# Optimization experiments

Measured on AMD Instinct MI355X. Metric: run time of the kernel, lower is better.

The kernel has to match this reference:

```python
import jax, jax.numpy as jnp
import numpy as np

# dims
D_IN, D, H, HD = 1536, 256, 8, 32
DEPTH, FFN = 2, 1024
B, L = 1, 8191
NGRIDS, TILE = 256, 256
SEGMENTS = [1024, 2048, 4096, 8192, 16384]   # get_optimal_segment_length(32768, 256)
RATIOS = [1, 2, 4, 8, 16]                    # LongNet canonical dilation ratios
SCALE = HD ** -0.5


def setup_inputs() -> dict:
    key = jax.random.key(0)
    ks = jax.random.split(key, 16)
    w = lambda k, s: jax.random.normal(k, s, jnp.float32) * 0.02
    return {
        "x": jax.random.normal(ks[0], (B, L, D_IN), jnp.float32),
        "coords": jax.random.randint(ks[1], (B, L, 2), 0, NGRIDS * TILE, jnp.int32),
        "proj_w": w(ks[2], (D_IN, D)), "proj_b": jnp.zeros((D,), jnp.float32),
        "cls_tok": w(ks[3], (1, 1, D)),
        "Wq": w(ks[4], (DEPTH, D, D)), "Wk": w(ks[5], (DEPTH, D, D)),
        "Wv": w(ks[6], (DEPTH, D, D)), "Wo": w(ks[7], (DEPTH, D, D)),
        "bq": jnp.zeros((DEPTH, D), jnp.float32), "bk": jnp.zeros((DEPTH, D), jnp.float32),
        "bv": jnp.zeros((DEPTH, D), jnp.float32), "bo": jnp.zeros((DEPTH, D), jnp.float32),
        "ln1_g": jnp.ones((DEPTH, D), jnp.float32), "ln1_b": jnp.zeros((DEPTH, D), jnp.float32),
        "ln2_g": jnp.ones((DEPTH, D), jnp.float32), "ln2_b": jnp.zeros((DEPTH, D), jnp.float32),
        "W1": w(ks[8], (DEPTH, D, FFN)), "b1": jnp.zeros((DEPTH, FFN), jnp.float32),
        "W2": w(ks[9], (DEPTH, FFN, D)), "b2": jnp.zeros((DEPTH, D), jnp.float32),
        "enc_g": jnp.ones((D,), jnp.float32), "enc_b": jnp.zeros((D,), jnp.float32),
        "norm_g": jnp.ones((D,), jnp.float32), "norm_b": jnp.zeros((D,), jnp.float32),
    }


def _ln(x, g, b):
    mu = x.mean(-1, keepdims=True)
    v = ((x - mu) ** 2).mean(-1, keepdims=True)
    return (x - mu) * jax.lax.rsqrt(v + 1e-5) * g + b


def _pos_table():
    # MAE-style 2D sincos pos embed, row 0 = cls (zeros). [NGRIDS^2+1, D]
    g = jnp.arange(NGRIDS, dtype=jnp.float32)
    gw, gh = jnp.meshgrid(g, g)  # gw[i,j]=j, gh[i,j]=i; flatten index = i*NGRIDS + j
    def one(pos):
        omega = 1.0 / (10000.0 ** (jnp.arange(D // 4, dtype=jnp.float32) / (D // 4)))
        o = pos.reshape(-1)[:, None] * omega[None]
        return jnp.concatenate([jnp.sin(o), jnp.cos(o)], -1)
    tab = jnp.concatenate([one(gw), one(gh)], -1)
    return jnp.concatenate([jnp.zeros((1, D), jnp.float32), tab], 0)


def _dilated_attn(q, k, v):
    # q,k,v: [B,S,H,HD]. LongNet: per (segment w, dilation r) branch, sparse in-segment
    # attention on stride-r rows (head-dependent offset h%r), branches fused via their
    # softmax log-sum-exp weights.
    S = q.shape[1]
    hh = jnp.arange(H)[:, None]
    outs, lses = [], []
    for w, r in zip(SEGMENTS, RATIOS):
        n = (S + w - 1) // w
        Sp = n * w
        def seg(t):
            tp = jnp.pad(t, ((0, 0), (0, Sp - S), (0, 0), (0, 0)))
            return tp.reshape(B, n, w, H, HD).transpose(0, 1, 3, 2, 4)  # [B,n,H,w,HD]
        qs_, ks_, vs_ = seg(q), seg(k), seg(v)
        t = w // r
        idx = (hh % r) + r * jnp.arange(t)[None, :]                  # [H,t]
        qs = qs_[:, :, hh, idx]                                      # [B,n,H,t,HD]
        ks = ks_[:, :, hh, idx]
        vs = vs_[:, :, hh, idx]
        valid = (jnp.arange(n)[:, None, None] * w + idx[None]) < S   # [n,H,t]
        sc = jnp.einsum('bnhtd,bnhsd->bnhts', qs, ks) * SCALE
        sc = jnp.where(valid[None, :, :, None, :], sc, -1e9)
        m = sc.max(-1, keepdims=True)
        p = jnp.exp(sc - m)
        den = p.sum(-1, keepdims=True)
        o = jnp.einsum('bnhts,bnhsd->bnhtd', p, vs) / den
        lse = m[..., 0] + jnp.log(den[..., 0])                       # [B,n,H,t]
        fo = jnp.zeros((B, n, H, w, HD), q.dtype).at[:, :, hh, idx].set(o)
        fl = jnp.full((B, n, H, w), -1e30, q.dtype).at[:, :, hh, idx].set(lse)
        outs.append(fo.transpose(0, 1, 3, 2, 4).reshape(B, Sp, H, HD)[:, :S])
        lses.append(fl.transpose(0, 1, 3, 2).reshape(B, Sp, H)[:, :S])
    Ls = jnp.stack(lses)   # [5,B,S,H]
    Os = jnp.stack(outs)   # [5,B,S,H,HD]
    wts = jnp.exp(Ls - Ls.max(0, keepdims=True))
    return (wts[..., None] * Os).sum(0) / wts.sum(0)[..., None]


def _forward(x, coords, proj_w, proj_b, cls_tok, Wq, Wk, Wv, Wo, bq, bk, bv, bo,
             ln1_g, ln1_b, ln2_g, ln2_b, W1, b1, W2, b2, enc_g, enc_b, norm_g, norm_b):
    h = x @ proj_w + proj_b                                   # patch embed [B,L,D]
    tab = _pos_table()
    cg = jnp.floor(coords.astype(jnp.float32) / TILE).astype(jnp.int32)
    pos = cg[..., 0] * NGRIDS + cg[..., 1] + 1                # coords_to_pos
    h = h + tab[pos]
    cls = jnp.broadcast_to(cls_tok + tab[0], (B, 1, D))
    h = jnp.concatenate([cls, h], 1)                          # [B,S,D], S = L+1
    S = h.shape[1]
    for i in range(DEPTH):                                    # pre-LN LongNet encoder layers
        a = _ln(h, ln1_g[i], ln1_b[i])
        q = (a @ Wq[i] + bq[i]).reshape(B, S, H, HD)
        k = (a @ Wk[i] + bk[i]).reshape(B, S, H, HD)
        v = (a @ Wv[i] + bv[i]).reshape(B, S, H, HD)
        o = _dilated_attn(q, k, v).reshape(B, S, D)
        h = h + o @ Wo[i] + bo[i]
        f = _ln(h, ln2_g[i], ln2_b[i])
        h = h + jax.nn.gelu(f @ W1[i] + b1[i], approximate=False) @ W2[i] + b2[i]
    h = _ln(h, enc_g, enc_b)     # encoder final LN
    h = _ln(h, norm_g, norm_b)   # model self.norm
    return h[:, 0]               # cls embedding (global_pool=False)


def reference(x, coords, proj_w, proj_b, cls_tok, Wq, Wk, Wv, Wo, bq, bk, bv, bo,
              ln1_g, ln1_b, ln2_g, ln2_b, W1, b1, W2, b2, enc_g, enc_b, norm_g, norm_b):
    return _forward(x, coords, proj_w, proj_b, cls_tok, Wq, Wk, Wv, Wo, bq, bk, bv, bo,
                    ln1_g, ln1_b, ln2_g, ln2_b, W1, b1, W2, b2, enc_g, enc_b, norm_g, norm_b)
```

## Files before the change

### kernel.cpp

```cpp
#include <hip/hip_runtime.h>
#include <math.h>

#define S_TOT 8192
#define DD 256
#define NHEAD 8
#define HDSZ 32
#define ATT_SCALE 0.17677669529663687f
#define ATT_SCALE_LOG2E 0.25506601f

typedef short short8 __attribute__((ext_vector_type(8)));
typedef short short4v __attribute__((ext_vector_type(4)));
typedef float f32x4 __attribute__((ext_vector_type(4)));
typedef unsigned short ushort;

#define OFF_PROJ 0
#define OFF_WQ0  393216
#define OFF_WK0  458752
#define OFF_WV0  524288
#define OFF_WO0  589824
#define OFF_W10  655360
#define OFF_W20  917504
#define OFF_WK1  1179648
#define OFF_WV1  1245184
#define OFF_WQ1  1310720
#define OFF_WO1  1376256
#define OFF_W11  1441792
#define OFF_W21  1703936
#define WBUF_TOT 1966080

__device__ inline ushort f2bf(float f) {
    union { float f; unsigned u; } c; c.f = f;
    unsigned u = c.u;
    u += 0x7fffu + ((u >> 16) & 1u);
    return (ushort)(u >> 16);
}
__device__ inline float bf2f(ushort u) {
    union { unsigned u; float f; } c; c.u = ((unsigned)u) << 16;
    return c.f;
}
__device__ inline float gelu_exact(float v) {
    return 0.5f * v * (1.0f + erff(v * 0.7071067811865475f));
}
__device__ inline unsigned cvtpk_bf16(float a, float b) {
    unsigned r;
    asm("v_cvt_pk_bf16_f32 %0, %1, %2" : "=v"(r) : "v"(a), "v"(b));
    return r;
}
__device__ inline short8 cat44(short4v a, short4v b) {
    return __builtin_shufflevector(a, b, 0, 1, 2, 3, 4, 5, 6, 7);
}
__device__ inline float block_sum256(float v, float* red) {
    #pragma unroll
    for (int off = 32; off > 0; off >>= 1) v += __shfl_down(v, off, 64);
    const int wid = threadIdx.x >> 6, lane = threadIdx.x & 63;
    if (lane == 0) red[wid] = v;
    __syncthreads();
    const float s = red[0] + red[1] + red[2] + red[3];
    __syncthreads();
    return s;
}

__global__ __launch_bounds__(256)
void setup_kernel(const float* __restrict__ x, const float* __restrict__ proj_w,
                  const float* __restrict__ Wq, const float* __restrict__ Wk,
                  const float* __restrict__ Wv, const float* __restrict__ Wo,
                  const float* __restrict__ W1, const float* __restrict__ W2,
                  const float* __restrict__ bq, const float* __restrict__ bk,
                  const float* __restrict__ bv, const float* __restrict__ cls_tok,
                  ushort* __restrict__ wbuf, float* __restrict__ bqkv0,
                  float* __restrict__ bkv1, ushort* __restrict__ xbf,
                  float* __restrict__ h)
{
    const int b = blockIdx.x;
    const int t = threadIdx.x;
    if (b >= 482) {
        if (b == 6626) { h[t] = cls_tok[t]; return; }
        const int i = (b - 482) * 256 + t;
        const int n8 = 8191 * 1536 / 8;
        if (i >= n8) return;
        const float4 a0 = *(const float4*)(x + (size_t)i * 8);
        const float4 a1 = *(const float4*)(x + (size_t)i * 8 + 4);
        ushort tmp[8] = { f2bf(a0.x), f2bf(a0.y), f2bf(a0.z), f2bf(a0.w),
                          f2bf(a1.x), f2bf(a1.y), f2bf(a1.z), f2bf(a1.w) };
        *(uint4*)(xbf + (size_t)i * 8) = *(const uint4*)tmp;
        return;
    }
    if (b >= 480) {
        if (b == 480) {
            for (int i = t; i < 768; i += 256)
                bqkv0[i] = (i < 256) ? bq[i] : ((i < 512) ? bk[i - 256] : bv[i - 512]);
        } else {
            for (int i = t; i < 512; i += 256)
                bkv1[i] = (i < 256) ? bk[256 + i] : bv[i];
        }
        return;
    }
    const float* src; ushort* dst; int R, C, t0;
    if (b < 96)       { src = proj_w;        dst = wbuf + OFF_PROJ; R = 1536; C = 256;  t0 = 0;   }
    else if (b < 112) { src = Wq;            dst = wbuf + OFF_WQ0;  R = 256;  C = 256;  t0 = 96;  }
    else if (b < 128) { src = Wk;            dst = wbuf + OFF_WK0;  R = 256;  C = 256;  t0 = 112; }
    else if (b < 144) { src = Wv;            dst = wbuf + OFF_WV0;  R = 256;  C = 256;  t0 = 128; }
    else if (b < 160) { src = Wo;            dst = wbuf + OFF_WO0;  R = 256;  C = 256;  t0 = 144; }
    else if (b < 224) { src = W1;            dst = wbuf + OFF_W10;  R = 256;  C = 1024; t0 = 160; }
    else if (b < 288) { src = W2;            dst = wbuf + OFF_W20;  R = 1024; C = 256;  t0 = 224; }
    else if (b < 304) { src = Wk + 65536;    dst = wbuf + OFF_WK1;  R = 256;  C = 256;  t0 = 288; }
    else if (b < 320) { src = Wv + 65536;    dst = wbuf + OFF_WV1;  R = 256;  C = 256;  t0 = 304; }
    else if (b < 336) { src = Wq + 65536;    dst = wbuf + OFF_WQ1;  R = 256;  C = 256;  t0 = 320; }
    else if (b < 352) { src = Wo + 65536;    dst = wbuf + OFF_WO1;  R = 256;  C = 256;  t0 = 336; }
    else if (b < 416) { src = W1 + 262144;   dst = wbuf + OFF_W11;  R = 256;  C = 1024; t0 = 352; }
    else              { src = W2 + 262144;   dst = wbuf + OFF_W21;  R = 1024; C = 256;  t0 = 416; }
    const int lt = b - t0;
    const int tC = C >> 6;
    const int tr = lt / tC, tc = lt % tC;
    __shared__ ushort tile[64][68];
    const int col = t & 63;
    const int r4  = t >> 6;
    #pragma unroll
    for (int i = 0; i < 16; ++i) {
        const int row = i * 4 + r4;
        tile[row][col] = f2bf(src[(size_t)(tr * 64 + row) * C + tc * 64 + col]);
    }
    __syncthreads();
    #pragma unroll
    for (int i = 0; i < 16; ++i) {
        const int n = i * 4 + r4;
        dst[(size_t)(tc * 64 + n) * R + tr * 64 + col] = tile[col][n];
    }
}

__global__ __launch_bounds__(256)
void ln_kernel(const float* __restrict__ in, const float* __restrict__ g,
               const float* __restrict__ b, ushort* __restrict__ outp)
{
    __shared__ float red[4];
    const int row = blockIdx.x;
    const int d = threadIdx.x;
    const float xv = in[(size_t)row * DD + d];
    const float mu = block_sum256(xv, red) * (1.0f / 256.0f);
    const float dv = xv - mu;
    const float var = block_sum256(dv * dv, red) * (1.0f / 256.0f);
    outp[(size_t)row * DD + d] = f2bf(dv * rsqrtf(var + 1e-5f) * g[d] + b[d]);
}

template <int BN>
__global__ __launch_bounds__(256)
void gemm4_kernel(const ushort* __restrict__ A, const ushort* __restrict__ Bt,
                  const float* __restrict__ bias, void* __restrict__ Cv,
                  int M, int N, int K, int flags, const int* __restrict__ coords)
{
    __shared__ ushort As[2][64][64];
    __shared__ ushort Bs[2][BN][64];
    constexpr int NT = BN / 32;
    const int nx  = N / BN;
    const int ny8 = gridDim.x / (8 * nx);
    const int b   = blockIdx.x;
    const int c8  = b & 7;
    const int j   = b >> 3;
    const int m0  = (c8 * ny8 + j / nx) * 64;
    const int n0  = (j % nx) * BN;

    const int tid  = threadIdx.x;
    const int wave = tid >> 6;
    const int lane = tid & 63;
    const int lrow = lane & 15;
    const int quad = lane >> 4;
    const int wr = (wave >> 1) * 32;
    const int wc = (wave & 1) * (BN / 2);

    float* Cf  = (float*)Cv;
    ushort* Cb = (ushort*)Cv;

    f32x4 acc[2][NT];
    #pragma unroll
    for (int mt = 0; mt < 2; ++mt)
        #pragma unroll
        for (int nt = 0; nt < NT; ++nt)
            acc[mt][nt] = (f32x4){0.f, 0.f, 0.f, 0.f};

    const int srow = tid >> 3;
    const int scol = (tid & 7) * 16;

    #define STAGE(BUF, KK)                                                        \
    do {                                                                          \
        _Pragma("unroll")                                                         \
        for (int c = 0; c < 2; ++c) {                                             \
            const int row = c * 32 + srow;                                        \
            const int sb  = scol ^ ((row & 7) << 4);                              \
            const ushort* srcp = A + (size_t)(m0 + row) * K + (KK) + (sb >> 1);   \
            __builtin_amdgcn_global_load_lds(                                     \
                (const __attribute__((address_space(1))) void*)srcp,              \
                (__attribute__((address_space(3))) void*)&As[BUF][c * 32 + wave * 8][0], \
                16, 0, 0);                                                        \
        }                                                                         \
        _Pragma("unroll")                                                         \
        for (int c = 0; c < BN / 32; ++c) {                                       \
            const int row = c * 32 + srow;                                        \
            const int sb  = scol ^ ((row & 7) << 4);                              \
            const ushort* srcp = Bt + (size_t)(n0 + row) * K + (KK) + (sb >> 1);  \
            __builtin_amdgcn_global_load_lds(                                     \
                (const __attribute__((address_space(1))) void*)srcp,              \
                (__attribute__((address_space(3))) void*)&Bs[BUF][c * 32 + wave * 8][0], \
                16, 0, 0);                                                        \
        }                                                                         \
    } while (0)

    int cur = 0;
    STAGE(0, 0);
    __syncthreads();
    for (int kk = 0; kk < K; kk += 64) {
        if (kk + 64 < K) STAGE(cur ^ 1, kk + 64);
        #pragma unroll
        for (int ks = 0; ks < 2; ++ks) {
            short8 af[2], bfr[NT];
            #pragma unroll
            for (int mt = 0; mt < 2; ++mt) {
                const int row = wr + mt * 16 + lrow;
                const int cb  = (ks * 64 + quad * 16) ^ ((row & 7) << 4);
                af[mt] = *(const short8*)((const char*)&As[cur][row][0] + cb);
            }
            #pragma unroll
            for (int nt = 0; nt < NT; ++nt) {
                const int row = wc + nt * 16 + lrow;
                const int cb  = (ks * 64 + quad * 16) ^ ((row & 7) << 4);
                bfr[nt] = *(const short8*)((const char*)&Bs[cur][row][0] + cb);
            }
            #pragma unroll
            for (int mt = 0; mt < 2; ++mt)
                #pragma unroll
                for (int nt = 0; nt < NT; ++nt)
                    acc[mt][nt] = __builtin_amdgcn_mfma_f32_16x16x32_bf16(
                                      af[mt], bfr[nt], acc[mt][nt], 0, 0, 0);
        }
        __syncthreads();
        cur ^= 1;
    }
    #undef STAGE

    #pragma unroll
    for (int mt = 0; mt < 2; ++mt) {
        #pragma unroll
        for (int rg = 0; rg < 4; ++rg) {
            const int r = m0 + wr + mt * 16 + quad * 4 + rg;
            if (r >= M) continue;
            #pragma unroll
            for (int nt = 0; nt < NT; ++nt) {
                const int c = n0 + wc + nt * 16 + lrow;
                float vv = acc[mt][nt][rg] + bias[c];
                if (flags & 8) {
                    const int cg = coords[2 * r + ((c < 128) ? 1 : 0)] >> 8;
                    const float omega = 1.0f / powf(10000.0f, (float)(c & 63) * (1.0f / 64.0f));
                    const float o = (float)cg * omega;
                    vv += ((c & 64) == 0) ? sinf(o) : cosf(o);
                }
                if (flags & 16) { if (c < 256) vv *= ATT_SCALE_LOG2E; }
                if (flags & 2) vv = gelu_exact(vv);
                if (flags & 4) {
                    Cb[(size_t)r * N + c] = f2bf(vv);
                } else {
                    if (flags & 1) vv += Cf[(size_t)r * N + c];
                    Cf[(size_t)r * N + c] = vv;
                }
            }
        }
    }
}

__global__ __launch_bounds__(256)
void attn_mfma_kernel(const ushort* __restrict__ q, const ushort* __restrict__ k,
                      const ushort* __restrict__ v, float* __restrict__ bo5,
                      float* __restrict__ lse5, int qs)
{
    __shared__ ushort Kb[2][64][40];
    __shared__ ushort Vt[2][32][72];

    const int unit = blockIdx.x;
    const int segu = unit >> 3;
    const int head = unit & 7;
    int b2, n;
    if (segu < 8)        { b2 = 0; n = segu; }
    else if (segu < 12)  { b2 = 1; n = segu - 8; }
    else if (segu < 14)  { b2 = 2; n = segu - 12; }
    else if (segu == 14) { b2 = 3; n = 0; }
    else                 { b2 = 4; n = 0; }
    const int w  = 1024 << b2;
    const int rr = 1 << b2;
    const int base = n * w + (head & (rr - 1));

    int kEnd = (S_TOT - base + rr - 1) >> b2;
    if (kEnd > 1024) kEnd = 1024;
    if (blockIdx.y * 128 >= kEnd) return;

    const int tid  = threadIdx.x;
    const int wave = tid >> 6;
    const int lane = tid & 63;
    const int lrow = lane & 15;
    const int quad = lane >> 4;

    short8 qf[2];
    #pragma unroll
    for (int m = 0; m < 2; ++m) {
        const int j  = blockIdx.y * 128 + wave * 32 + m * 16 + lrow;
        const int pq = base + rr * j;
        qf[m] = *(const short8*)(q + (size_t)pq * qs + head * HDSZ + quad * 8);
    }

    f32x4 acc[2][2];
    float lsum[2] = {0.f, 0.f};
    #pragma unroll
    for (int m = 0; m < 2; ++m)
        #pragma unroll
        for (int dt = 0; dt < 2; ++dt) acc[m][dt] = (f32x4){0.f, 0.f, 0.f, 0.f};

    const int skr = tid >> 2;
    const int sdb = (tid & 3) * 8;
    const int grp = tid & 3;
    const int wcol = (2 * skr + 32 * grp) & 127;

    size_t prow = (size_t)(base + rr * skr) * qs + head * HDSZ + sdb;
    uint4 kreg = *(const uint4*)(k + prow);
    uint4 vreg = *(const uint4*)(v + prow);

    *(uint4*)&Kb[0][skr][sdb] = kreg;
    {
        const ushort* vp = (const ushort*)&vreg;
        #pragma unroll
        for (int i = 0; i < 8; ++i)
            *(ushort*)((char*)&Vt[0][sdb + i][0] + wcol) = vp[i];
    }

    int cur = 0;
    for (int kc = 0; kc < kEnd; kc += 64) {
        __syncthreads();
        const bool more = (kc + 64 < kEnd);
        if (more) {
            prow = (size_t)(base + rr * (kc + 64 + skr)) * qs + head * HDSZ + sdb;
            kreg = *(const uint4*)(k + prow);
            vreg = *(const uint4*)(v + prow);
        }

        short8 kf[4];
        #pragma unroll
        for (int t = 0; t < 4; ++t)
            kf[t] = *(const short8*)&Kb[cur][t * 16 + lrow][quad * 8];

        short8 vf[2][2];
        #pragma unroll
        for (int g = 0; g < 2; ++g)
            #pragma unroll
            for (int dt = 0; dt < 2; ++dt) {
                const int row  = dt * 16 + lrow;
                const int rotb = 32 * ((row >> 3) & 3);
                const int cb0  = (64 * g + 8 * quad + rotb) & 127;
                const int cb1  = (64 * g + 8 * quad + 32 + rotb) & 127;
                vf[g][dt] = cat44(*(const short4v*)((const char*)&Vt[cur][row][0] + cb0),
                                  *(const short4v*)((const char*)&Vt[cur][row][0] + cb1));
            }

        #pragma unroll
        for (int m = 0; m < 2; ++m) {
            f32x4 sc[4];
            #pragma unroll
            for (int t = 0; t < 4; ++t)
                sc[t] = __builtin_amdgcn_mfma_f32_16x16x32_bf16(
                            kf[t], qf[m], (f32x4){0.f,0.f,0.f,0.f}, 0, 0, 0);
            float p[4][4];
            #pragma unroll
            for (int t = 0; t < 4; ++t)
                #pragma unroll
                for (int rg = 0; rg < 4; ++rg)
                    p[t][rg] = exp2f(sc[t][rg]);
            float ps = 0.f;
            #pragma unroll
            for (int t = 0; t < 4; ++t)
                ps += (p[t][0] + p[t][1]) + (p[t][2] + p[t][3]);
            lsum[m] += ps;
            unsigned pw[4][2];
            #pragma unroll
            for (int t = 0; t < 4; ++t) {
                pw[t][0] = cvtpk_bf16(p[t][0], p[t][1]);
                pw[t][1] = cvtpk_bf16(p[t][2], p[t][3]);
            }
            #pragma unroll
            for (int g = 0; g < 2; ++g) {
                union { short8 s; unsigned u[4]; } pa;
                pa.u[0] = pw[2 * g][0];
                pa.u[1] = pw[2 * g][1];
                pa.u[2] = pw[2 * g + 1][0];
                pa.u[3] = pw[2 * g + 1][1];
                #pragma unroll
                for (int dt = 0; dt < 2; ++dt)
                    acc[m][dt] = __builtin_amdgcn_mfma_f32_16x16x32_bf16(
                                     pa.s, vf[g][dt], acc[m][dt], 0, 0, 0);
            }
        }

        if (more) {
            *(uint4*)&Kb[cur ^ 1][skr][sdb] = kreg;
            const ushort* vp = (const ushort*)&vreg;
            #pragma unroll
            for (int i = 0; i < 8; ++i)
                *(ushort*)((char*)&Vt[cur ^ 1][sdb + i][0] + wcol) = vp[i];
        }
        cur ^= 1;
    }

    #pragma unroll
    for (int m = 0; m < 2; ++m) {
        float tot = lsum[m];
        tot += __shfl_xor(tot, 16, 64);
        tot += __shfl_xor(tot, 32, 64);
        #pragma unroll
        for (int rg = 0; rg < 4; ++rg) {
            const float li = __shfl(tot, quad * 4 + rg, 16);
            const int j  = blockIdx.y * 128 + wave * 32 + m * 16 + quad * 4 + rg;
            const int pq = base + rr * j;
            const float inv = 1.0f / li;
            float* dst = bo5 + ((size_t)b2 * S_TOT + pq) * DD + head * HDSZ;
            dst[lrow]      = acc[m][0][rg] * inv;
            dst[16 + lrow] = acc[m][1][rg] * inv;
            if (lrow == 0)
                lse5[((size_t)b2 * S_TOT + pq) * NHEAD + head] = __logf(li);
        }
    }
}

__global__ __launch_bounds__(64)
void attn_row0_kernel(const float* __restrict__ q, const ushort* __restrict__ k,
                      const ushort* __restrict__ v, float* __restrict__ bo5,
                      float* __restrict__ lse5, int kvs)
{
    const int b2 = blockIdx.x >> 3;
    const int head = blockIdx.x & 7;
    const int r = 1 << b2;
    if (head & (r - 1)) return;
    const int tid = threadIdx.x;
    float qreg[32];
    #pragma unroll
    for (int d = 0; d < 32; d += 4) {
        const float4 t4 = *(const float4*)(q + head * HDSZ + d);
        qreg[d] = t4.x; qreg[d+1] = t4.y; qreg[d+2] = t4.z; qreg[d+3] = t4.w;
    }
    float m = -3.0e38f, l = 0.f, o[32];
    #pragma unroll
    for (int d = 0; d < 32; ++d) o[d] = 0.f;
    for (int j = tid; j < 1024; j += 64) {
        const int pk = r * j;
        float s;
        if (pk < S_TOT) {
            float s0 = 0.f;
            #pragma unroll
            for (int d = 0; d < 32; d += 8) {
                const uint4 raw = *(const uint4*)(k + (size_t)pk * kvs + head * HDSZ + d);
                const ushort* kp = (const ushort*)&raw;
                #pragma unroll
                for (int i = 0; i < 8; ++i) s0 += qreg[d + i] * bf2f(kp[i]);
            }
            s = s0 * ATT_SCALE;
        } else s = -1.0e9f;
        const float mn = fmaxf(m, s);
        const float c = __expf(m - mn);
        const float e = __expf(s - mn);
        l = l * c + e; m = mn;
        if (pk < S_TOT) {
            #pragma unroll
            for (int d = 0; d < 32; d += 8) {
                const uint4 raw = *(const uint4*)(v + (size_t)pk * kvs + head * HDSZ + d);
                const ushort* vp = (const ushort*)&raw;
                #pragma unroll
                for (int i = 0; i < 8; ++i) o[d + i] = o[d + i] * c + e * bf2f(vp[i]);
            }
        } else {
            #pragma unroll
            for (int d = 0; d < 32; ++d) o[d] *= c;
        }
    }
    __shared__ float ms[64], ls[64], os[64][32];
    ms[tid] = m; ls[tid] = l;
    #pragma unroll
    for (int d = 0; d < 32; ++d) os[tid][d] = o[d];
    __syncthreads();
    for (int st = 32; st >= 1; st >>= 1) {
        if (tid < st) {
            const float m2 = ms[tid + st], l2 = ls[tid + st];
            const float mn = fmaxf(ms[tid], m2);
            const float c1 = __expf(ms[tid] - mn);
            const float c2 = __expf(m2 - mn);
            ls[tid] = ls[tid] * c1 + l2 * c2;
            ms[tid] = mn;
            for (int d = 0; d < 32; ++d) os[tid][d] = os[tid][d]*c1 + os[tid+st][d]*c2;
        }
        __syncthreads();
    }
    if (tid < 32) bo5[(size_t)b2 * S_TOT * DD + head * HDSZ + tid] = os[0][tid] / ls[0];
    if (tid == 0) lse5[(size_t)b2 * S_TOT * NHEAD + head] = ms[0] + __logf(ls[0]);
}

__global__ __launch_bounds__(256)
void combine_kernel(const float* __restrict__ bo5, const float* __restrict__ lse5,
                    ushort* __restrict__ attn)
{
    const int p = blockIdx.x;
    const int d = threadIdx.x;
    const int h = d >> 5;
    float lse[5];
    bool sel[5];
    float mx = -3.0e38f;
    #pragma unroll
    for (int b2 = 0; b2 < 5; ++b2) {
        const int r = 1 << b2;
        sel[b2] = ((p & (r - 1)) == (h & (r - 1)));
        if (sel[b2]) {
            lse[b2] = lse5[((size_t)b2 * S_TOT + p) * NHEAD + h];
            mx = fmaxf(mx, lse[b2]);
        }
    }
    float wsum = 0.f, acc = 0.f;
    #pragma unroll
    for (int b2 = 0; b2 < 5; ++b2) {
        if (sel[b2]) {
            const float wgt = __expf(lse[b2] - mx);
            wsum += wgt;
            acc += wgt * bo5[((size_t)b2 * S_TOT + p) * DD + d];
        }
    }
    attn[(size_t)p * DD + d] = f2bf(acc / wsum);
}

__global__ __launch_bounds__(256)
void tail_qrow_kernel(const float* __restrict__ h, const float* __restrict__ g,
                      const float* __restrict__ b, const ushort* __restrict__ Wt,
                      const float* __restrict__ bias, float* __restrict__ qrow0)
{
    __shared__ float red[4];
    __shared__ float as[256];
    const int d = threadIdx.x;
    const float xv = h[d];
    const float mu = block_sum256(xv, red) * (1.0f / 256.0f);
    const float dv = xv - mu;
    const float var = block_sum256(dv * dv, red) * (1.0f / 256.0f);
    as[d] = dv * rsqrtf(var + 1e-5f) * g[d] + b[d];
    __syncthreads();
    float acc = 0.f;
    for (int k2 = 0; k2 < 256; k2 += 8) {
        const short8 w8 = *(const short8*)&Wt[(size_t)d * 256 + k2];
        #pragma unroll
        for (int j = 0; j < 8; ++j) acc += as[k2 + j] * bf2f((ushort)w8[j]);
    }
    qrow0[d] = acc + bias[d];
}

__global__ __launch_bounds__(256)
void tail_mid_kernel(const float* __restrict__ bo5, const float* __restrict__ lse5,
                     float* __restrict__ h, const ushort* __restrict__ Wo1t,
                     const float* __restrict__ bo1, const float* __restrict__ g2,
                     const float* __restrict__ b2, float* __restrict__ f)
{
    __shared__ float red[4];
    __shared__ float att[256];
    const int d = threadIdx.x;
    const int hh = d >> 5;
    float lse[5]; bool sel[5]; float mx = -3.0e38f;
    #pragma unroll
    for (int bb = 0; bb < 5; ++bb) {
        const int r = 1 << bb;
        sel[bb] = ((hh & (r - 1)) == 0);
        if (sel[bb]) {
            lse[bb] = lse5[(size_t)bb * S_TOT * NHEAD + hh];
            mx = fmaxf(mx, lse[bb]);
        }
    }
    float wsum = 0.f, acc = 0.f;
    #pragma unroll
    for (int bb = 0; bb < 5; ++bb) {
        if (sel[bb]) {
            const float wgt = __expf(lse[bb] - mx);
            wsum += wgt;
            acc += wgt * bo5[(size_t)bb * S_TOT * DD + d];
        }
    }
    att[d] = acc / wsum;
    __syncthreads();
    float a2 = 0.f;
    for (int k2 = 0; k2 < 256; k2 += 8) {
        const short8 w8 = *(const short8*)&Wo1t[(size_t)d * 256 + k2];
        #pragma unroll
        for (int j = 0; j < 8; ++j) a2 += att[k2 + j] * bf2f((ushort)w8[j]);
    }
    const float hv = a2 + bo1[d] + h[d];
    h[d] = hv;
    const float mu = block_sum256(hv, red) * (1.0f / 256.0f);
    const float dv = hv - mu;
    const float var = block_sum256(dv * dv, red) * (1.0f / 256.0f);
    f[d] = dv * rsqrtf(var + 1e-5f) * g2[d] + b2[d];
}

__global__ __launch_bounds__(256)
void tail_ffn1_kernel(const float* __restrict__ f, const ushort* __restrict__ W11t,
                      const float* __restrict__ b11, float* __restrict__ midr0)
{
    __shared__ float fs[256];
    const int tid = threadIdx.x;
    fs[tid] = f[tid];
    __syncthreads();
    const int n = blockIdx.x * 256 + tid;
    float acc = 0.f;
    for (int k2 = 0; k2 < 256; k2 += 8) {
        const short8 w8 = *(const short8*)&W11t[(size_t)n * 256 + k2];
        #pragma unroll
        for (int j = 0; j < 8; ++j) acc += fs[k2 + j] * bf2f((ushort)w8[j]);
    }
    midr0[n] = gelu_exact(acc + b11[n]);
}

__global__ __launch_bounds__(256)
void tail_ffn2_kernel(const float* __restrict__ midr0, const ushort* __restrict__ W21t,
                      const float* __restrict__ b21, float* __restrict__ h)
{
    __shared__ float ms[1024];
    const int tid = threadIdx.x;
    for (int i = tid; i < 1024; i += 256) ms[i] = midr0[i];
    __syncthreads();
    const int n  = blockIdx.x * 64 + (tid >> 2);
    const int kq = (tid & 3) * 256;
    float acc = 0.f;
    for (int k2 = 0; k2 < 256; k2 += 8) {
        const short8 w8 = *(const short8*)&W21t[(size_t)n * 1024 + kq + k2];
        #pragma unroll
        for (int j = 0; j < 8; ++j) acc += ms[kq + k2 + j] * bf2f((ushort)w8[j]);
    }
    acc += __shfl_xor(acc, 1);
    acc += __shfl_xor(acc, 2);
    if ((tid & 3) == 0) h[n] = h[n] + acc + b21[n];
}

__global__ __launch_bounds__(256)
void tail_final_kernel(const float* __restrict__ h, const float* __restrict__ eg,
                       const float* __restrict__ eb, const float* __restrict__ ng,
                       const float* __restrict__ nb, float* __restrict__ out)
{
    __shared__ float red[4];
    const int d = threadIdx.x;
    float xv = h[d];
    {
        const float mu = block_sum256(xv, red) * (1.0f / 256.0f);
        const float dv = xv - mu;
        const float var = block_sum256(dv * dv, red) * (1.0f / 256.0f);
        xv = dv * rsqrtf(var + 1e-5f) * eg[d] + eb[d];
    }
    {
        const float mu = block_sum256(xv, red) * (1.0f / 256.0f);
        const float dv = xv - mu;
        const float var = block_sum256(dv * dv, red) * (1.0f / 256.0f);
        out[d] = dv * rsqrtf(var + 1e-5f) * ng[d] + nb[d];
    }
}

extern "C" void kernel_launch(void* const* d_in, const int* in_sizes, int n_in,
                              void* d_out, int out_size, void* d_ws, size_t ws_size,
                              hipStream_t stream)
{
    const float* x      = (const float*)d_in[0];
    const int*   coords = (const int*)  d_in[1];
    const float* proj_w = (const float*)d_in[2];
    const float* proj_b = (const float*)d_in[3];
    const float* cls_tok= (const float*)d_in[4];
    const float* Wq     = (const float*)d_in[5];
    const float* Wk     = (const float*)d_in[6];
    const float* Wv     = (const float*)d_in[7];
    const float* Wo     = (const float*)d_in[8];
    const float* bq     = (const float*)d_in[9];
    const float* bk     = (const float*)d_in[10];
    const float* bv     = (const float*)d_in[11];
    const float* bo_    = (const float*)d_in[12];
    const float* ln1_g  = (const float*)d_in[13];
    const float* ln1_b  = (const float*)d_in[14];
    const float* ln2_g  = (const float*)d_in[15];
    const float* ln2_b  = (const float*)d_in[16];
    const float* W1     = (const float*)d_in[17];
    const float* b1     = (const float*)d_in[18];
    const float* W2     = (const float*)d_in[19];
    const float* b2v    = (const float*)d_in[20];
    const float* enc_g  = (const float*)d_in[21];
    const float* enc_b  = (const float*)d_in[22];
    const float* norm_g = (const float*)d_in[23];
    const float* norm_b = (const float*)d_in[24];
    float* out = (float*)d_out;

    const size_t SD = (size_t)S_TOT * DD;
    float* ws   = (float*)d_ws;
    float* h    = ws;
    float* big  = h + SD;
    float* bo5  = big;
    ushort* xbf   = (ushort*)big;
    ushort* midbf = (ushort*)big;
    float* lse5 = big + 5 * SD;
    ushort* a_bf    = (ushort*)(lse5 + 5 * S_TOT * NHEAD);
    ushort* qkv_bf  = a_bf + SD;
    ushort* attn_bf = qkv_bf + 3 * SD;
    ushort* wbuf    = attn_bf + SD;
    float* bqkv0  = (float*)(wbuf + WBUF_TOT);
    float* bkv1   = bqkv0 + 768;
    float* qrow0  = bkv1 + 512;
    float* f_r0   = qrow0 + 256;
    float* midr0  = f_r0 + 256;

    auto gemm64 = [&](const ushort* A, const ushort* Bt, const float* bias, void* C,
                      int M, int N, int K, int flags) {
        gemm4_kernel<64><<<128 * (N / 64), 256, 0, stream>>>(A, Bt, bias, C, M, N, K,
                                                             flags, coords);
    };
    auto gemm128 = [&](const ushort* A, const ushort* Bt, const float* bias, void* C,
                       int M, int N, int K, int flags) {
        gemm4_kernel<128><<<128 * (N / 128), 256, 0, stream>>>(A, Bt, bias, C, M, N, K,
                                                               flags, coords);
    };

    setup_kernel<<<6627, 256, 0, stream>>>(x, proj_w, Wq, Wk, Wv, Wo, W1, W2,
                                           bq, bk, bv, cls_tok, wbuf, bqkv0, bkv1,
                                           xbf, h);

    gemm64(xbf, wbuf + OFF_PROJ, proj_b, h + DD, 8191, 256, 1536, 8);

    ln_kernel<<<S_TOT, 256, 0, stream>>>(h, ln1_g, ln1_b, a_bf);
    gemm128(a_bf, wbuf + OFF_WQ0, bqkv0, qkv_bf, 8192, 768, 256, 4 | 16);
    attn_mfma_kernel<<<dim3(128, 8), 256, 0, stream>>>(qkv_bf, qkv_bf + 256,
                                                       qkv_bf + 512, bo5, lse5, 768);
    combine_kernel<<<S_TOT, 256, 0, stream>>>(bo5, lse5, attn_bf);
    gemm64(attn_bf, wbuf + OFF_WO0, bo_, h, 8192, 256, 256, 1);
    ln_kernel<<<S_TOT, 256, 0, stream>>>(h, ln2_g, ln2_b, a_bf);
    gemm128(a_bf, wbuf + OFF_W10, b1, midbf, 8192, 1024, 256, 4 | 2);
    gemm64(midbf, wbuf + OFF_W20, b2v, h, 8192, 256, 1024, 1);

    ln_kernel<<<S_TOT, 256, 0, stream>>>(h, ln1_g + 256, ln1_b + 256, a_bf);
    gemm128(a_bf, wbuf + OFF_WK1, bkv1, qkv_bf, 8192, 512, 256, 4);
    tail_qrow_kernel<<<1, 256, 0, stream>>>(h, ln1_g + 256, ln1_b + 256,
                                            wbuf + OFF_WQ1, bq + 256, qrow0);
    attn_row0_kernel<<<40, 64, 0, stream>>>(qrow0, qkv_bf, qkv_bf + 256, bo5, lse5, 512);
    tail_mid_kernel<<<1, 256, 0, stream>>>(bo5, lse5, h, wbuf + OFF_WO1, bo_ + 256,
                                           ln2_g + 256, ln2_b + 256, f_r0);
    tail_ffn1_kernel<<<4, 256, 0, stream>>>(f_r0, wbuf + OFF_W11, b1 + 1024, midr0);
    tail_ffn2_kernel<<<4, 256, 0, stream>>>(midr0, wbuf + OFF_W21, b2v + 256, h);
    tail_final_kernel<<<1, 256, 0, stream>>>(h, enc_g, enc_b, norm_g, norm_b, out);
}
```

Baseline: 432.7 us.

## Triple-buffer GEMM k-loop with vmcnt waits, use BN=64 everywhere, fast sincos

Changes the GEMM main loop from double buffering with __syncthreads to a three-stage LDS ring. Loads are issued two tiles ahead, and each step waits with an explicit s_waitcnt vmcnt plus s_barrier, so global-to-LDS transfers overlap more of the compute. All GEMMs that used the 128-wide N tile now use the 64-wide tile, which gives more blocks. The positional-embedding epilogue replaces powf/sinf/cosf with exp2f and the fast __sinf/__cosf intrinsics. This costs more shared memory per block and lowers accuracy of the sincos terms, because the arguments can be large.

```diff
diff --git a/kernel.cpp b/kernel.cpp
--- a/kernel.cpp
+++ b/kernel.cpp
@@ -148,8 +148,8 @@
                   const float* __restrict__ bias, void* __restrict__ Cv,
                   int M, int N, int K, int flags, const int* __restrict__ coords)
 {
-    __shared__ ushort As[2][64][64];
-    __shared__ ushort Bs[2][BN][64];
+    __shared__ ushort As[3][64][64];
+    __shared__ ushort Bs[3][BN][64];
     constexpr int NT = BN / 32;
     const int nx  = N / BN;
     const int ny8 = gridDim.x / (8 * nx);
@@ -204,37 +204,59 @@
         }                                                                         \
     } while (0)
 
-    int cur = 0;
+    #define COMPUTE(BUF)                                                          \
+    do {                                                                          \
+        _Pragma("unroll")                                                         \
+        for (int ks = 0; ks < 2; ++ks) {                                          \
+            short8 af[2], bfr[NT];                                                \
+            _Pragma("unroll")                                                     \
+            for (int mt = 0; mt < 2; ++mt) {                                      \
+                const int row = wr + mt * 16 + lrow;                              \
+                const int cb  = (ks * 64 + quad * 16) ^ ((row & 7) << 4);         \
+                af[mt] = *(const short8*)((const char*)&As[BUF][row][0] + cb);    \
+            }                                                                     \
+            _Pragma("unroll")                                                     \
+            for (int nt = 0; nt < NT; ++nt) {                                     \
+                const int row = wc + nt * 16 + lrow;                              \
+                const int cb  = (ks * 64 + quad * 16) ^ ((row & 7) << 4);         \
+                bfr[nt] = *(const short8*)((const char*)&Bs[BUF][row][0] + cb);   \
+            }                                                                     \
+            _Pragma("unroll")                                                     \
+            for (int mt = 0; mt < 2; ++mt)                                        \
+                _Pragma("unroll")                                                 \
+                for (int nt = 0; nt < NT; ++nt)                                   \
+                    acc[mt][nt] = __builtin_amdgcn_mfma_f32_16x16x32_bf16(        \
+                                      af[mt], bfr[nt], acc[mt][nt], 0, 0, 0);     \
+        }                                                                         \
+    } while (0)
+
+    #define WAIT_BAR(NVM)                                                         \
+    do {                                                                          \
+        asm volatile("s_waitcnt vmcnt(" #NVM ")" ::: "memory");                   \
+        __builtin_amdgcn_sched_barrier(0);                                        \
+        __builtin_amdgcn_s_barrier();                                             \
+        __builtin_amdgcn_sched_barrier(0);                                        \
+    } while (0)
+
+    const int ktiles = K >> 6;
     STAGE(0, 0);
-    __syncthreads();
-    for (int kk = 0; kk < K; kk += 64) {
-        if (kk + 64 < K) STAGE(cur ^ 1, kk + 64);
-        #pragma unroll
-        for (int ks = 0; ks < 2; ++ks) {
-            short8 af[2], bfr[NT];
-            #pragma unroll
-            for (int mt = 0; mt < 2; ++mt) {
-                const int row = wr + mt * 16 + lrow;
-                const int cb  = (ks * 64 + quad * 16) ^ ((row & 7) << 4);
-                af[mt] = *(const short8*)((const char*)&As[cur][row][0] + cb);
-            }
-            #pragma unroll
-            for (int nt = 0; nt < NT; ++nt) {
-                const int row = wc + nt * 16 + lrow;
-                const int cb  = (ks * 64 + quad * 16) ^ ((row & 7) << 4);
-                bfr[nt] = *(const short8*)((const char*)&Bs[cur][row][0] + cb);
-            }
-            #pragma unroll
-            for (int mt = 0; mt < 2; ++mt)
-                #pragma unroll
-                for (int nt = 0; nt < NT; ++nt)
-                    acc[mt][nt] = __builtin_amdgcn_mfma_f32_16x16x32_bf16(
-                                      af[mt], bfr[nt], acc[mt][nt], 0, 0, 0);
-        }
-        __syncthreads();
-        cur ^= 1;
-    }
+    STAGE(1, 64);
+    int bt = 0;
+    for (int t = 0; t < ktiles - 2; ++t) {
+        WAIT_BAR(4);
+        const int nb = (bt + 2 >= 3) ? bt - 1 : bt + 2;
+        STAGE(nb, (t + 2) * 64);
+        COMPUTE(bt);
+        bt = (bt + 1 == 3) ? 0 : bt + 1;
+    }
+    WAIT_BAR(4);
+    COMPUTE(bt);
+    bt = (bt + 1 == 3) ? 0 : bt + 1;
+    WAIT_BAR(0);
+    COMPUTE(bt);
     #undef STAGE
+    #undef COMPUTE
+    #undef WAIT_BAR
 
     #pragma unroll
     for (int mt = 0; mt < 2; ++mt) {
@@ -248,9 +270,9 @@
                 float vv = acc[mt][nt][rg] + bias[c];
                 if (flags & 8) {
                     const int cg = coords[2 * r + ((c < 128) ? 1 : 0)] >> 8;
-                    const float omega = 1.0f / powf(10000.0f, (float)(c & 63) * (1.0f / 64.0f));
+                    const float omega = exp2f((float)(c & 63) * -0.2076205059304703f);
                     const float o = (float)cg * omega;
-                    vv += ((c & 64) == 0) ? sinf(o) : cosf(o);
+                    vv += ((c & 64) == 0) ? __sinf(o) : __cosf(o);
                 }
                 if (flags & 16) { if (c < 256) vv *= ATT_SCALE_LOG2E; }
                 if (flags & 2) vv = gelu_exact(vv);
@@ -709,11 +731,6 @@
         gemm4_kernel<64><<<128 * (N / 64), 256, 0, stream>>>(A, Bt, bias, C, M, N, K,
                                                              flags, coords);
     };
-    auto gemm128 = [&](const ushort* A, const ushort* Bt, const float* bias, void* C,
-                       int M, int N, int K, int flags) {
-        gemm4_kernel<128><<<128 * (N / 128), 256, 0, stream>>>(A, Bt, bias, C, M, N, K,
-                                                               flags, coords);
-    };
 
     setup_kernel<<<6627, 256, 0, stream>>>(x, proj_w, Wq, Wk, Wv, Wo, W1, W2,
                                            bq, bk, bv, cls_tok, wbuf, bqkv0, bkv1,
@@ -722,17 +739,17 @@
     gemm64(xbf, wbuf + OFF_PROJ, proj_b, h + DD, 8191, 256, 1536, 8);
 
     ln_kernel<<<S_TOT, 256, 0, stream>>>(h, ln1_g, ln1_b, a_bf);
-    gemm128(a_bf, wbuf + OFF_WQ0, bqkv0, qkv_bf, 8192, 768, 256, 4 | 16);
+    gemm64(a_bf, wbuf + OFF_WQ0, bqkv0, qkv_bf, 8192, 768, 256, 4 | 16);
     attn_mfma_kernel<<<dim3(128, 8), 256, 0, stream>>>(qkv_bf, qkv_bf + 256,
                                                        qkv_bf + 512, bo5, lse5, 768);
     combine_kernel<<<S_TOT, 256, 0, stream>>>(bo5, lse5, attn_bf);
     gemm64(attn_bf, wbuf + OFF_WO0, bo_, h, 8192, 256, 256, 1);
     ln_kernel<<<S_TOT, 256, 0, stream>>>(h, ln2_g, ln2_b, a_bf);
-    gemm128(a_bf, wbuf + OFF_W10, b1, midbf, 8192, 1024, 256, 4 | 2);
+    gemm64(a_bf, wbuf + OFF_W10, b1, midbf, 8192, 1024, 256, 4 | 2);
     gemm64(midbf, wbuf + OFF_W20, b2v, h, 8192, 256, 1024, 1);
 
     ln_kernel<<<S_TOT, 256, 0, stream>>>(h, ln1_g + 256, ln1_b + 256, a_bf);
-    gemm128(a_bf, wbuf + OFF_WK1, bkv1, qkv_bf, 8192, 512, 256, 4);
+    gemm64(a_bf, wbuf + OFF_WK1, bkv1, qkv_bf, 8192, 512, 256, 4);
     tail_qrow_kernel<<<1, 256, 0, stream>>>(h, ln1_g + 256, ln1_b + 256,
                                             wbuf + OFF_WQ1, bq + 256, qrow0);
     attn_row0_kernel<<<40, 64, 0, stream>>>(qrow0, qkv_bf, qkv_bf + 256, bo5, lse5, 512);
```

Result: faster. 379.4 us (-12.3%).
